# Kernel optimization log

Hardware: AMD Instinct MI355X
Metric: run time of the kernel (lower is better)

Reference implementation:

```python
import jax, jax.numpy as jnp
import numpy as np
from jax import lax

D_MODEL, D_STATE, DT_RANK, D_INNER, K = 96, 16, 6, 192, 4


def cross_scan(x):
    # x: (B, C, H, W) -> (B, 4, C, L)
    B, C, H, W = x.shape
    x0 = x.reshape(B, C, H * W)                         # row-major scan
    x1 = jnp.transpose(x, (0, 1, 3, 2)).reshape(B, C, H * W)  # column-major scan
    return jnp.stack([x0, x1, x0[..., ::-1], x1[..., ::-1]], axis=1)


def cross_merge(ys, H, W):
    # ys: (B, 4, D, L) -> (B, D, L)
    B, Kd, D, L = ys.shape
    ys = ys[:, 0:2] + ys[:, 2:4, :, ::-1]
    y1 = jnp.transpose(ys[:, 1].reshape(B, D, W, H), (0, 1, 3, 2)).reshape(B, D, L)
    return ys[:, 0] + y1


def selective_scan(u, delta, A, Bs, Cs, Ds, delta_bias):
    # u, delta: (B, K, D, L); A: (K, D, N); Bs, Cs: (B, K, N, L); Ds, delta_bias: (K, D)
    Bsz, Kd, Dm, L = u.shape
    N = A.shape[-1]
    delta = jax.nn.softplus(delta + delta_bias[None, :, :, None])
    du = delta * u
    d_l = jnp.moveaxis(delta, -1, 0)   # (L, B, K, D)
    du_l = jnp.moveaxis(du, -1, 0)
    b_l = jnp.moveaxis(Bs, -1, 0)      # (L, B, K, N)
    c_l = jnpp = jnp.moveaxis(Cs, -1, 0)

    def step(h, inp):
        d_t, du_t, b_t, c_t = inp
        h = jnp.exp(d_t[..., None] * A) * h + du_t[..., None] * b_t[:, :, None, :]
        y = jnp.einsum('bkdn,bkn->bkd', h, c_t)
        return h, y

    h0 = jnp.zeros((Bsz, Kd, Dm, N), u.dtype)
    _, ys = lax.scan(step, h0, (d_l, du_l, b_l, c_l))
    ys = jnp.moveaxis(ys, 0, -1)  # (B, K, D, L)
    return ys + Ds[None, :, :, None] * u


def _forward(x, in_proj_w, conv_w, conv_b, x_proj_w, dt_projs_w, dt_projs_b,
             A_logs, Ds, out_norm_w, out_norm_b, out_proj_w):
    Bsz, H, W, dm = x.shape
    d_in = conv_w.shape[0]
    R, N = dt_projs_w.shape[2], A_logs.shape[-1]
    L = H * W
    # in_proj (no bias), split into x and gate z
    xz = jnp.einsum('bhwc,oc->bhwo', x, in_proj_w)
    xpart, z = jnp.split(xz, 2, axis=-1)
    z = jax.nn.silu(z)
    # depthwise 3x3 conv (NCHW) + SiLU
    xc = jnp.transpose(xpart, (0, 3, 1, 2))
    xc = lax.conv_general_dilated(xc, conv_w, (1, 1), 'SAME',
                                  feature_group_count=d_in,
                                  dimension_numbers=('NCHW', 'OIHW', 'NCHW'))
    xc = jax.nn.silu(xc + conv_b[None, :, None, None])
    # 4-directional cross scan
    xs = cross_scan(xc)                                   # (B, 4, d_in, L)
    x_dbl = jnp.einsum('bkdl,kcd->bkcl', xs, x_proj_w)    # (B, 4, R+2N, L)
    dts = jnp.einsum('bkrl,kdr->bkdl', x_dbl[:, :, :R], dt_projs_w)
    Bs = x_dbl[:, :, R:R + N]
    Cs = x_dbl[:, :, R + N:]
    A = -jnp.exp(A_logs)                                  # (4, d_in, N)
    ys = selective_scan(xs, dts, A, Bs, Cs, Ds, dt_projs_b)
    y = cross_merge(ys, H, W)                             # (B, d_in, L)
    y = jnp.transpose(y.reshape(Bsz, d_in, H, W), (0, 2, 3, 1))
    # out_norm = LayerNorm(d_inner), eps=1e-5
    mu = y.mean(-1, keepdims=True)
    var = ((y - mu) ** 2).mean(-1, keepdims=True)
    y = (y - mu) / jnp.sqrt(var + 1e-5) * out_norm_w + out_norm_b
    y = y * z
    return jnp.einsum('bhwd,od->bhwo', y, out_proj_w)


def setup_inputs() -> dict:
    key = jax.random.key(0)
    ks = jax.random.split(key, 8)
    dm, d_in, N, R = D_MODEL, D_INNER, D_STATE, DT_RANK
    x = jax.random.normal(ks[0], (8, 64, 64, dm), jnp.float32)
    in_proj_w = jax.random.normal(ks[1], (2 * d_in, dm), jnp.float32) * 0.02
    conv_w = jax.random.normal(ks[2], (d_in, 1, 3, 3), jnp.float32) * 0.1
    conv_b = jnp.zeros((d_in,), jnp.float32)
    x_proj_w = jax.random.normal(ks[3], (K, R + 2 * N, d_in), jnp.float32) * 0.02
    dt_projs_w = jax.random.normal(ks[4], (K, d_in, R), jnp.float32) * 0.1
    dt_projs_b = jax.random.uniform(ks[5], (K, d_in), jnp.float32, minval=-4.0, maxval=-2.0)
    A_logs = jnp.log(jnp.tile(jnp.arange(1, N + 1, dtype=jnp.float32)[None, None, :], (K, d_in, 1)))
    Ds = jnp.ones((K, d_in), jnp.float32)
    out_norm_w = jnp.ones((d_in,), jnp.float32)
    out_norm_b = jnp.zeros((d_in,), jnp.float32)
    out_proj_w = jax.random.normal(ks[6], (dm, d_in), jnp.float32) * 0.02
    return dict(x=x, in_proj_w=in_proj_w, conv_w=conv_w, conv_b=conv_b,
                x_proj_w=x_proj_w, dt_projs_w=dt_projs_w, dt_projs_b=dt_projs_b,
                A_logs=A_logs, Ds=Ds, out_norm_w=out_norm_w, out_norm_b=out_norm_b,
                out_proj_w=out_proj_w)


def reference(x, in_proj_w, conv_w, conv_b, x_proj_w, dt_projs_w, dt_projs_b,
              A_logs, Ds, out_norm_w, out_norm_b, out_proj_w):
    return _forward(x, in_proj_w, conv_w, conv_b, x_proj_w, dt_projs_w, dt_projs_b,
                    A_logs, Ds, out_norm_w, out_norm_b, out_proj_w)
```

## Files before the change

### kernel.cpp

```cpp
#include <hip/hip_runtime.h>
#include <math.h>

#define B_SZ 8
#define Hh 64
#define Ww 64
#define L 4096
#define Dm 96
#define Din 192
#define Kd 4
#define Ns 16
#define CPROJ 38
#define ROWW 40
#define NCHUNK 128
#define CHUNK 32

__device__ __forceinline__ float siluf_(float x){ return x / (1.f + __expf(-x)); }

__global__ void prep_kernel(const float* __restrict__ inw,
                            const float* __restrict__ xpw,
                            const float* __restrict__ outw,
                            float* __restrict__ wt_in,
                            float* __restrict__ wt_x,
                            float* __restrict__ wt_out){
  int i = blockIdx.x * blockDim.x + threadIdx.x;
  if (i < Dm*2*Din){ int k = i/(2*Din); int o = i%(2*Din); wt_in[i] = inw[o*Dm + k]; }
  int j = i - Dm*2*Din;
  if (j >= 0 && j < Din*Kd*CPROJ){ int k = j/(Kd*CPROJ); int c = j%(Kd*CPROJ); wt_x[j] = xpw[c*Din + k]; }
  int l = j - Din*Kd*CPROJ;
  if (l >= 0 && l < Din*Dm){ int dd = l/Dm; int o = l%Dm; wt_out[l] = outw[o*Din + dd]; }
}

__global__ __launch_bounds__(256) void zero_kernel(float4* __restrict__ p, int n4){
  int i = blockIdx.x * 256 + threadIdx.x;
  if (i < n4) p[i] = make_float4(0.f,0.f,0.f,0.f);
}

template<int KDIM, int OREAL, int EPI>
__global__ __launch_bounds__(256) void gemm_kernel(const float* __restrict__ X,
    const float* __restrict__ W, float* __restrict__ out0, float* __restrict__ out1){
  __shared__ float4 xt[128*24];
  const int tid = threadIdx.x;
  const int pg = tid & 15, og = tid >> 4;
  const int pblk = blockIdx.x & 255;
  const int oblk = blockIdx.x >> 8;
  const int p0 = pblk * 128;
  const bool act = (oblk*128 + og*8) < OREAL;
  int oc = oblk*128 + og*8;
  if (oc > OREAL-8) oc = OREAL-8;
  const int sw = pg & 7;

  float acc[8][8];
  #pragma unroll
  for (int i=0;i<8;i++){
    #pragma unroll
    for (int j2=0;j2<8;j2++) acc[i][j2] = 0.f;
  }

  for (int kp = 0; kp < KDIM/96; ++kp){
    __syncthreads();
    for (int idx = tid; idx < 128*24; idx += 256){
      int pp = idx/24, k4 = idx%24;
      size_t prow;
      if (EPI == 1){
        int b = pblk >> 5, tau = pblk & 31;
        int h = ((tau>>2)<<3) + (pp>>4);
        int w = ((tau&3)<<4) + (pp&15);
        prow = (size_t)b*L + h*64 + w;
      } else prow = (size_t)p0 + pp;
      float4 v = *(const float4*)&X[prow*KDIM + (size_t)kp*96 + k4*4];
      xt[pp*24 + (k4 ^ (pp&7))] = v;
    }
    __syncthreads();

    if (act){
      for (int k4 = 0; k4 < 24; ++k4){
        float4 wv[8];
        #pragma unroll
        for (int kk=0;kk<4;kk++){
          const float* wr = &W[(size_t)(kp*96 + k4*4 + kk)*OREAL + oc];
          wv[kk*2]   = *(const float4*)wr;
          wv[kk*2+1] = *(const float4*)(wr+4);
        }
        float4 xv[8];
        #pragma unroll
        for (int i=0;i<8;i++) xv[i] = xt[(pg+16*i)*24 + (k4 ^ sw)];
        #pragma unroll
        for (int kk=0;kk<4;kk++){
          const float4 wa = wv[kk*2], wb = wv[kk*2+1];
          #pragma unroll
          for (int i=0;i<8;i++){
            const float xk = ((const float*)&xv[i])[kk];
            acc[i][0] += xk*wa.x; acc[i][1] += xk*wa.y; acc[i][2] += xk*wa.z; acc[i][3] += xk*wa.w;
            acc[i][4] += xk*wb.x; acc[i][5] += xk*wb.y; acc[i][6] += xk*wb.z; acc[i][7] += xk*wb.w;
          }
        }
      }
    }
  }

  if (!act) return;
  if (EPI == 0){
    #pragma unroll
    for (int i=0;i<8;i++){
      size_t p = (size_t)p0 + pg + 16*i;
      if (oc < Din){
        *(float4*)&out0[p*Din + oc]     = make_float4(acc[i][0],acc[i][1],acc[i][2],acc[i][3]);
        *(float4*)&out0[p*Din + oc + 4] = make_float4(acc[i][4],acc[i][5],acc[i][6],acc[i][7]);
      } else {
        int zo = oc - Din;
        *(float4*)&out1[p*Din + zo]     = make_float4(siluf_(acc[i][0]),siluf_(acc[i][1]),siluf_(acc[i][2]),siluf_(acc[i][3]));
        *(float4*)&out1[p*Din + zo + 4] = make_float4(siluf_(acc[i][4]),siluf_(acc[i][5]),siluf_(acc[i][6]),siluf_(acc[i][7]));
      }
    }
  } else if (EPI == 1){
    const int b = pblk >> 5, tau = pblk & 31;
    #pragma unroll
    for (int i=0;i<8;i++){
      int q = pg + 16*i;
      int h = ((tau>>2)<<3) + (q>>4);
      int w = ((tau&3)<<4) + (q&15);
      int hw = h*64 + w;
      int t1 = ((hw&63)<<6) | (hw>>6);
      #pragma unroll
      for (int j2=0;j2<8;j2++){
        int c = oc + j2;
        int kd = c / CPROJ; int cc = c - kd*CPROJ;
        int t = (kd==0)? hw : (kd==1)? t1 : (kd==2)? (L-1-hw) : (L-1-t1);
        int dcol = (cc < 6) ? (32+cc) : (cc-6);
        out0[((size_t)(b*Kd+kd)*L + t)*ROWW + dcol] = acc[i][j2];
      }
    }
  } else {
    #pragma unroll
    for (int i=0;i<8;i++){
      size_t p = (size_t)p0 + pg + 16*i;
      *(float4*)&out0[p*Dm + oc]     = make_float4(acc[i][0],acc[i][1],acc[i][2],acc[i][3]);
      *(float4*)&out0[p*Dm + oc + 4] = make_float4(acc[i][4],acc[i][5],acc[i][6],acc[i][7]);
    }
  }
}

__global__ __launch_bounds__(256) void conv_kernel(const float* __restrict__ xp,
    const float* __restrict__ cw, const float* __restrict__ cb, float* __restrict__ u){
  const int gid = blockIdx.x * 256 + threadIdx.x;
  const int d = gid % Din; const int p = gid / Din;
  const int b = p / L; const int hw = p % L; const int h = hw >> 6; const int w = hw & 63;
  float acc = cb[d];
  #pragma unroll
  for (int i=-1;i<=1;i++){
    const int hh = h + i; if (hh < 0 || hh >= Hh) continue;
    #pragma unroll
    for (int j=-1;j<=1;j++){
      const int ww = w + j; if (ww < 0 || ww >= Ww) continue;
      acc += xp[((size_t)(b*L + hh*Ww + ww))*Din + d] * cw[d*9 + (i+1)*3 + (j+1)];
    }
  }
  u[(size_t)p*Din + d] = siluf_(acc);
}

__device__ __forceinline__ void affine_pos(int k, int t0, int& gp0, int& gstr){
  if (k == 0){ gp0 = t0; gstr = 1; }
  else if (k == 1){ gp0 = ((t0 & 63) << 6) | (t0 >> 6); gstr = 64; }
  else if (k == 2){ gp0 = L-1-t0; gstr = -1; }
  else { const int T0 = L-1-t0; gp0 = ((T0 & 63) << 6) | (T0 >> 6); gstr = -64; }
}

__device__ __forceinline__ void ladder_(float e1, float* e){
  e[0]=e1;
  #pragma unroll
  for (int n=1;n<16;n++){ int P=n+1; e[n] = e[(P+1)/2 - 1] * e[P/2 - 1]; }
}

__device__ __forceinline__ float scan_step(const float* __restrict__ row, float uval,
    const float* __restrict__ wdt, float bias, const float* __restrict__ a2,
    bool fast, float* __restrict__ hst){
  float dr = bias;
  #pragma unroll
  for (int r=0;r<6;r++) dr += row[32+r]*wdt[r];
  const float p = __expf(dr);
  const float delta = (dr > 20.f) ? dr : __logf(1.f + p);
  const float du = delta * uval;
  float e[16];
  if (fast){
    ladder_(1.f/(1.f + p), e);
  } else {
    #pragma unroll
    for (int n=0;n<16;n++) e[n] = __expf(delta * a2[n]);
  }
  #pragma unroll
  for (int n=0;n<16;n++) hst[n] = e[n]*hst[n] + du*row[n];
  return delta;
}

__device__ __forceinline__ float ydot_(const float* __restrict__ hst,
    const float* __restrict__ row){
  float ya=0.f,yb=0.f,yc=0.f,yd=0.f;
  #pragma unroll
  for (int n=0;n<16;n+=4){
    ya += hst[n]*row[16+n];   yb += hst[n+1]*row[17+n];
    yc += hst[n+2]*row[18+n]; yd += hst[n+3]*row[19+n];
  }
  return (ya+yb)+(yc+yd);
}

__global__ __launch_bounds__(192) void scanq_kernel(const float* __restrict__ u,
    const float* __restrict__ xq, const float* __restrict__ dtw,
    const float* __restrict__ dtb, const float* __restrict__ alog,
    float* __restrict__ qout, float* __restrict__ Sout){
  const int bid = blockIdx.x;
  const int c = bid & (NCHUNK-1); const int k = (bid >> 7) & 3; const int b = bid >> 9;
  const int d = threadIdx.x;
  const int bk = b*Kd + k;
  float wdt[6];
  #pragma unroll
  for (int r=0;r<6;r++) wdt[r] = dtw[(k*Din + d)*6 + r];
  const float bias = dtb[k*Din + d];
  float a2[16]; bool fastb = true;
  #pragma unroll
  for (int n=0;n<16;n++){
    a2[n] = -__expf(alog[(k*Din + d)*16 + n]);
    fastb = fastb && (fabsf(a2[n] + (float)(n+1)) < 1e-5f*(float)(n+1));
  }
  const bool fast = (bool)__all((int)fastb);
  float hst[16];
  #pragma unroll
  for (int n=0;n<16;n++) hst[n] = 0.f;
  float S = 0.f;
  const int t0 = c * CHUNK;
  int gp0, gstr; affine_pos(k, t0, gp0, gstr);
  const float* __restrict__ up = u + (size_t)b*L*Din + (size_t)gp0*Din + d;
  const ptrdiff_t ustep = (ptrdiff_t)gstr * Din;
  const float* __restrict__ rowp = xq + ((size_t)bk*L + t0)*ROWW;
  for (int s = 0; s < CHUNK; ++s){
    S += scan_step(rowp, *up, wdt, bias, a2, fast, hst);
    up += ustep; rowp += ROWW;
  }
  const size_t base = ((size_t)bk*NCHUNK + c)*Ns*Din + d;
  #pragma unroll
  for (int n=0;n<16;n++) qout[base + (size_t)n*Din] = hst[n];
  Sout[((size_t)bk*NCHUNK + c)*Din + d] = S;
}

__global__ __launch_bounds__(256) void combine_kernel(const float* __restrict__ alog,
    float* __restrict__ q, const float* __restrict__ Sin){
  const int gid = blockIdx.x * 256 + threadIdx.x;
  if (gid >= B_SZ*Kd*Ns*Din) return;
  const int d = gid % Din; const int n = (gid / Din) % Ns; const int bk = gid / (Din*Ns);
  const int k = bk & 3;
  const float A = -__expf(alog[(k*Din + d)*16 + n]);
  float h = 0.f;
  for (int c=0;c<NCHUNK;c++){
    const size_t idx = (((size_t)bk*NCHUNK + c)*Ns + n)*Din + d;
    const float qv = q[idx];
    q[idx] = h;
    h = __expf(A * Sin[((size_t)bk*NCHUNK + c)*Din + d]) * h + qv;
  }
}

__global__ __launch_bounds__(192) void scany_kernel(const float* __restrict__ u,
    const float* __restrict__ xq, const float* __restrict__ dtw,
    const float* __restrict__ dtb, const float* __restrict__ alog,
    const float* __restrict__ Dsin, const float* __restrict__ hin,
    float* __restrict__ ym){
  const int bid = blockIdx.x;
  const int c = bid & (NCHUNK-1); const int k = (bid >> 7) & 3; const int b = bid >> 9;
  const int d = threadIdx.x;
  const int bk = b*Kd + k;

  float wdt[6];
  #pragma unroll
  for (int r=0;r<6;r++) wdt[r] = dtw[(k*Din + d)*6 + r];
  const float bias = dtb[k*Din + d];
  const float Dval = Dsin[k*Din + d];
  float a2[16]; bool fastb = true;
  #pragma unroll
  for (int n=0;n<16;n++){
    a2[n] = -__expf(alog[(k*Din + d)*16 + n]);
    fastb = fastb && (fabsf(a2[n] + (float)(n+1)) < 1e-5f*(float)(n+1));
  }
  const bool fast = (bool)__all((int)fastb);
  float hst[16];
  const size_t hbase = ((size_t)bk*NCHUNK + c)*Ns*Din + d;
  #pragma unroll
  for (int n=0;n<16;n++) hst[n] = hin[hbase + (size_t)n*Din];

  const int t0 = c * CHUNK;
  int gp0, gstr; affine_pos(k, t0, gp0, gstr);
  const float* __restrict__ up = u + (size_t)b*L*Din + (size_t)gp0*Din + d;
  float* __restrict__ yp = ym + (size_t)b*L*Din + (size_t)gp0*Din + d;
  const ptrdiff_t ustep = (ptrdiff_t)gstr * Din;
  const float* __restrict__ rowp = xq + ((size_t)bk*L + t0)*ROWW;
  for (int s = 0; s < CHUNK; ++s){
    const float uval = *up;
    scan_step(rowp, uval, wdt, bias, a2, fast, hst);
    atomicAdd(yp, ydot_(hst, rowp) + Dval*uval);
    up += ustep; yp += ustep; rowp += ROWW;
  }
}

__global__ __launch_bounds__(192) void lnz_kernel(const float* __restrict__ ym,
    const float* __restrict__ z,
    const float* __restrict__ gw, const float* __restrict__ gb,
    float* __restrict__ yg){
  __shared__ float red[2][4];
  const int p = blockIdx.x;
  const int d = threadIdx.x;
  const size_t i = (size_t)p*Din + d;
  const float yv = ym[i];
  float s = yv, ss = yv*yv;
  #pragma unroll
  for (int off=32; off>=1; off>>=1){ s += __shfl_down(s, off); ss += __shfl_down(ss, off); }
  const int wave = d >> 6;
  if ((d & 63) == 0){ red[0][wave] = s; red[1][wave] = ss; }
  __syncthreads();
  const float mu = (red[0][0]+red[0][1]+red[0][2]) * (1.f/Din);
  const float var = (red[1][0]+red[1][1]+red[1][2]) * (1.f/Din) - mu*mu;
  const float inv = rsqrtf(var + 1e-5f);
  yg[i] = ((yv - mu)*inv*gw[d] + gb[d]) * z[i];
}

extern "C" void kernel_launch(void* const* d_in, const int* in_sizes, int n_in,
                              void* d_out, int out_size, void* d_ws, size_t ws_size,
                              hipStream_t stream) {
  const float* x      = (const float*)d_in[0];
  const float* inw    = (const float*)d_in[1];
  const float* convw  = (const float*)d_in[2];
  const float* convb  = (const float*)d_in[3];
  const float* xprojw = (const float*)d_in[4];
  const float* dtw    = (const float*)d_in[5];
  const float* dtb    = (const float*)d_in[6];
  const float* alog   = (const float*)d_in[7];
  const float* Ds     = (const float*)d_in[8];
  const float* gw     = (const float*)d_in[9];
  const float* gb     = (const float*)d_in[10];
  const float* outw   = (const float*)d_in[11];
  float* out = (float*)d_out;

  float* ws = (float*)d_ws;
  const size_t nBLD  = (size_t)B_SZ*L*Din;
  const size_t nXQ   = (size_t)B_SZ*Kd*L*ROWW;
  const size_t nQ    = (size_t)B_SZ*Kd*NCHUNK*Ns*Din;
  const size_t nS    = (size_t)B_SZ*Kd*NCHUNK*Din;
  size_t off = 0;
  float* xpart = ws + off; off += nBLD;
  float* zbuf  = ws + off; off += nBLD;
  float* ubuf  = ws + off; off += nBLD;
  float* xq    = ws + off; off += nXQ;
  float* qbuf  = ws + off; off += nQ;
  float* Sbuf  = ws + off; off += nS;
  float* ym    = ws + off; off += nBLD;
  float* wt_in = ws + off; off += (size_t)Dm*2*Din;
  float* wt_x  = ws + off; off += (size_t)Din*Kd*CPROJ;
  float* wt_out= ws + off; off += (size_t)Din*Dm;

  const int prepN = Dm*2*Din + Din*Kd*CPROJ + Din*Dm;
  prep_kernel<<<(prepN + 255)/256, 256, 0, stream>>>(inw, xprojw, outw, wt_in, wt_x, wt_out);
  zero_kernel<<<(int)(nBLD/4 + 255)/256, 256, 0, stream>>>((float4*)ym, (int)(nBLD/4));
  gemm_kernel<Dm, 2*Din, 0><<<256*3, 256, 0, stream>>>(x, wt_in, xpart, zbuf);
  conv_kernel<<<(int)(nBLD/256), 256, 0, stream>>>(xpart, convw, convb, ubuf);
  gemm_kernel<Din, Kd*CPROJ, 1><<<256*2, 256, 0, stream>>>(ubuf, wt_x, xq, nullptr);
  scanq_kernel<<<B_SZ*Kd*NCHUNK, Din, 0, stream>>>(ubuf, xq, dtw, dtb, alog, qbuf, Sbuf);
  combine_kernel<<<(B_SZ*Kd*Ns*Din + 255)/256, 256, 0, stream>>>(alog, qbuf, Sbuf);
  scany_kernel<<<B_SZ*Kd*NCHUNK, Din, 0, stream>>>(ubuf, xq, dtw, dtb, alog, Ds, qbuf, ym);
  lnz_kernel<<<B_SZ*L, Din, 0, stream>>>(ym, zbuf, gw, gb, qbuf);
  gemm_kernel<Din, Dm, 2><<<256*1, 256, 0, stream>>>(qbuf, wt_out, out, nullptr);
}
```

Measured before the change: 501.4 us.

## Fuse layernorm-gate into out-projection kernel and vectorize scan row loads

Fuses the LayerNorm, z-gating and output projection into one kernel that stages normalized rows in swizzled shared memory, which removes the separate lnz pass and the intermediate buffer round trip. The scan kernels now load B/C/dt rows as float4 vectors, unroll the time loop and use a hardware reciprocal. The combine step writes prefix states to the reused xpart buffer instead of updating in place. The old scany_kernel is left with garbled, dead code that is never launched, and the workspace layout is resized to fit.

```diff
diff --git a/kernel.cpp b/kernel.cpp
--- a/kernel.cpp
+++ b/kernel.cpp
@@ -112,7 +112,7 @@
         *(float4*)&out1[p*Din + zo + 4] = make_float4(siluf_(acc[i][4]),siluf_(acc[i][5]),siluf_(acc[i][6]),siluf_(acc[i][7]));
       }
     }
-  } else if (EPI == 1){
+  } else {
     const int b = pblk >> 5, tau = pblk & 31;
     #pragma unroll
     for (int i=0;i<8;i++){
@@ -130,13 +130,6 @@
         out0[((size_t)(b*Kd+kd)*L + t)*ROWW + dcol] = acc[i][j2];
       }
     }
-  } else {
-    #pragma unroll
-    for (int i=0;i<8;i++){
-      size_t p = (size_t)p0 + pg + 16*i;
-      *(float4*)&out0[p*Dm + oc]     = make_float4(acc[i][0],acc[i][1],acc[i][2],acc[i][3]);
-      *(float4*)&out0[p*Dm + oc + 4] = make_float4(acc[i][4],acc[i][5],acc[i][6],acc[i][7]);
-    }
   }
 }
 
@@ -169,38 +162,6 @@
   e[0]=e1;
   #pragma unroll
   for (int n=1;n<16;n++){ int P=n+1; e[n] = e[(P+1)/2 - 1] * e[P/2 - 1]; }
-}
-
-__device__ __forceinline__ float scan_step(const float* __restrict__ row, float uval,
-    const float* __restrict__ wdt, float bias, const float* __restrict__ a2,
-    bool fast, float* __restrict__ hst){
-  float dr = bias;
-  #pragma unroll
-  for (int r=0;r<6;r++) dr += row[32+r]*wdt[r];
-  const float p = __expf(dr);
-  const float delta = (dr > 20.f) ? dr : __logf(1.f + p);
-  const float du = delta * uval;
-  float e[16];
-  if (fast){
-    ladder_(1.f/(1.f + p), e);
-  } else {
-    #pragma unroll
-    for (int n=0;n<16;n++) e[n] = __expf(delta * a2[n]);
-  }
-  #pragma unroll
-  for (int n=0;n<16;n++) hst[n] = e[n]*hst[n] + du*row[n];
-  return delta;
-}
-
-__device__ __forceinline__ float ydot_(const float* __restrict__ hst,
-    const float* __restrict__ row){
-  float ya=0.f,yb=0.f,yc=0.f,yd=0.f;
-  #pragma unroll
-  for (int n=0;n<16;n+=4){
-    ya += hst[n]*row[16+n];   yb += hst[n+1]*row[17+n];
-    yc += hst[n+2]*row[18+n]; yd += hst[n+3]*row[19+n];
-  }
-  return (ya+yb)+(yc+yd);
 }
 
 __global__ __launch_bounds__(192) void scanq_kernel(const float* __restrict__ u,
@@ -222,38 +183,59 @@
     fastb = fastb && (fabsf(a2[n] + (float)(n+1)) < 1e-5f*(float)(n+1));
   }
   const bool fast = (bool)__all((int)fastb);
-  float hst[16];
-  #pragma unroll
-  for (int n=0;n<16;n++) hst[n] = 0.f;
+  float h[16];
+  #pragma unroll
+  for (int n=0;n<16;n++) h[n] = 0.f;
   float S = 0.f;
   const int t0 = c * CHUNK;
   int gp0, gstr; affine_pos(k, t0, gp0, gstr);
   const float* __restrict__ up = u + (size_t)b*L*Din + (size_t)gp0*Din + d;
   const ptrdiff_t ustep = (ptrdiff_t)gstr * Din;
   const float* __restrict__ rowp = xq + ((size_t)bk*L + t0)*ROWW;
+  #pragma unroll 4
   for (int s = 0; s < CHUNK; ++s){
-    S += scan_step(rowp, *up, wdt, bias, a2, fast, hst);
+    const float4* __restrict__ rq = (const float4*)rowp;
+    const float4 B0=rq[0],B1=rq[1],B2=rq[2],B3=rq[3];
+    const float4 D0=rq[8];
+    const float2 D1=((const float2*)rowp)[18];
+    const float uval = *up;
+    float dr = bias + D0.x*wdt[0]+D0.y*wdt[1]+D0.z*wdt[2]+D0.w*wdt[3]+D1.x*wdt[4]+D1.y*wdt[5];
+    const float pp = __expf(dr);
+    const float delta = (dr > 20.f) ? dr : __logf(1.f + pp);
+    S += delta;
+    const float du = delta * uval;
+    float e[16];
+    if (fast){
+      ladder_(__builtin_amdgcn_rcpf(1.f + pp), e);
+    } else {
+      #pragma unroll
+      for (int n=0;n<16;n++) e[n] = __expf(delta * a2[n]);
+    }
+    h[0] =e[0] *h[0] +du*B0.x; h[1] =e[1] *h[1] +du*B0.y; h[2] =e[2] *h[2] +du*B0.z; h[3] =e[3] *h[3] +du*B0.w;
+    h[4] =e[4] *h[4] +du*B1.x; h[5] =e[5] *h[5] +du*B1.y; h[6] =e[6] *h[6] +du*B1.z; h[7] =e[7] *h[7] +du*B1.w;
+    h[8] =e[8] *h[8] +du*B2.x; h[9] =e[9] *h[9] +du*B2.y; h[10]=e[10]*h[10]+du*B2.z; h[11]=e[11]*h[11]+du*B2.w;
+    h[12]=e[12]*h[12]+du*B3.x; h[13]=e[13]*h[13]+du*B3.y; h[14]=e[14]*h[14]+du*B3.z; h[15]=e[15]*h[15]+du*B3.w;
     up += ustep; rowp += ROWW;
   }
   const size_t base = ((size_t)bk*NCHUNK + c)*Ns*Din + d;
   #pragma unroll
-  for (int n=0;n<16;n++) qout[base + (size_t)n*Din] = hst[n];
+  for (int n=0;n<16;n++) qout[base + (size_t)n*Din] = h[n];
   Sout[((size_t)bk*NCHUNK + c)*Din + d] = S;
 }
 
 __global__ __launch_bounds__(256) void combine_kernel(const float* __restrict__ alog,
-    float* __restrict__ q, const float* __restrict__ Sin){
+    const float* __restrict__ qin, const float* __restrict__ Sin, float* __restrict__ hout){
   const int gid = blockIdx.x * 256 + threadIdx.x;
   if (gid >= B_SZ*Kd*Ns*Din) return;
   const int d = gid % Din; const int n = (gid / Din) % Ns; const int bk = gid / (Din*Ns);
   const int k = bk & 3;
   const float A = -__expf(alog[(k*Din + d)*16 + n]);
   float h = 0.f;
+  #pragma unroll 2
   for (int c=0;c<NCHUNK;c++){
     const size_t idx = (((size_t)bk*NCHUNK + c)*Ns + n)*Din + d;
-    const float qv = q[idx];
-    q[idx] = h;
-    h = __expf(A * Sin[((size_t)bk*NCHUNK + c)*Din + d]) * h + qv;
+    hout[idx] = h;
+    h = __expf(A * Sin[((size_t)bk*NCHUNK + c)*Din + d]) * h + qin[idx];
   }
 }
 
@@ -279,10 +261,10 @@
     fastb = fastb && (fabsf(a2[n] + (float)(n+1)) < 1e-5f*(float)(n+1));
   }
   const bool fast = (bool)__all((int)fastb);
-  float hst[16];
+  float h[16];
   const size_t hbase = ((size_t)bk*NCHUNK + c)*Ns*Din + d;
   #pragma unroll
-  for (int n=0;n<16;n++) hst[n] = hin[hbase + (size_t)n*Din];
+  for (int n=0;n<16;n++) h[n] = hin[hbase + (size_t)n*Din];
 
   const int t0 = c * CHUNK;
   int gp0, gstr; affine_pos(k, t0, gp0, gstr);
@@ -290,33 +272,175 @@
   float* __restrict__ yp = ym + (size_t)b*L*Din + (size_t)gp0*Din + d;
   const ptrdiff_t ustep = (ptrdiff_t)gstr * Din;
   const float* __restrict__ rowp = xq + ((size_t)bk*L + t0)*ROWW;
+  #pragma unroll 4
   for (int s = 0; s < CHUNK; ++s){
+    const float4* __restrict__ rq = (const float4*)rowp;
+    const float4 B0=rq[0],B1=rq[1],B2=rq[2],B3=rq[3];
+    const float4 C0=rq[4],C1=rq[5],C2=rq[6],C3=rq[7];
+    const float4 D0=rq[8];
+    const float2 D1=((const float2*)rowp)[18];
     const float uval = *up;
-    scan_step(rowp, uval, wdt, bias, a2, fast, hst);
-    atomicAdd(yp, ydot_(hst, rowp) + Dval*uval);
+    float dr = bias + D0.x*wdt[0]+D0.y*wdt[1]+D0.z*wdt[2]+D0.w*wdt[3]+D1.x*wdt[4]+D1.y*wdt[5];
+    const float pp = __expf(dr);
+    const float delta = (dr > 20.f) ? dr : __logf(1.f + pp);
+    const float du = delta * uval;
+    float e[16];
+    if (fast){
+      ladder_(__builtin_amdgcn_rcpf(1.f + pp), e);
+    } else {
+      #pragma unroll
+      for (int n=0;n<16;n++) e[n] = __expf(delta * a2[n]);
+    }
+    h[0] =e[0] *h[0] +du*B0.x; h[1] =e[1] *h[1] +du*B0.y; h[2] =e[2] *h[2] +du*B0.z; h[3] =e[3] *h[3] +du*B0.w;
+    h[4] =e[4] *h[4] +du*B1.x; h[5] =e[5] *h[5] +du*B1.y; h[6] =e[6] *h[6] +du*B1.z; h[7] =e[7] *h[7] +du*B1.w;
+    h[8] =e[8] *h[8] +du*B2.x; h[9] =e[9] *h[9] +du*B2.z==0.f?h[9]:e[9]*h[9]+du*B2.y;
+    h[9] =e[9] *h[9];
     up += ustep; yp += ustep; rowp += ROWW;
   }
 }
 
-__global__ __launch_bounds__(192) void lnz_kernel(const float* __restrict__ ym,
-    const float* __restrict__ z,
-    const float* __restrict__ gw, const float* __restrict__ gb,
-    float* __restrict__ yg){
-  __shared__ float red[2][4];
-  const int p = blockIdx.x;
+__global__ __launch_bounds__(192) void scany_kernel2(const float* __restrict__ u,
+    const float* __restrict__ xq, const float* __restrict__ dtw,
+    const float* __restrict__ dtb, const float* __restrict__ alog,
+    const float* __restrict__ Dsin, const float* __restrict__ hin,
+    float* __restrict__ ym){
+  const int bid = blockIdx.x;
+  const int c = bid & (NCHUNK-1); const int k = (bid >> 7) & 3; const int b = bid >> 9;
   const int d = threadIdx.x;
-  const size_t i = (size_t)p*Din + d;
-  const float yv = ym[i];
-  float s = yv, ss = yv*yv;
-  #pragma unroll
-  for (int off=32; off>=1; off>>=1){ s += __shfl_down(s, off); ss += __shfl_down(ss, off); }
-  const int wave = d >> 6;
-  if ((d & 63) == 0){ red[0][wave] = s; red[1][wave] = ss; }
+  const int bk = b*Kd + k;
+
+  float wdt[6];
+  #pragma unroll
+  for (int r=0;r<6;r++) wdt[r] = dtw[(k*Din + d)*6 + r];
+  const float bias = dtb[k*Din + d];
+  const float Dval = Dsin[k*Din + d];
+  float a2[16]; bool fastb = true;
+  #pragma unroll
+  for (int n=0;n<16;n++){
+    a2[n] = -__expf(alog[(k*Din + d)*16 + n]);
+    fastb = fastb && (fabsf(a2[n] + (float)(n+1)) < 1e-5f*(float)(n+1));
+  }
+  const bool fast = (bool)__all((int)fastb);
+  float h[16];
+  const size_t hbase = ((size_t)bk*NCHUNK + c)*Ns*Din + d;
+  #pragma unroll
+  for (int n=0;n<16;n++) h[n] = hin[hbase + (size_t)n*Din];
+
+  const int t0 = c * CHUNK;
+  int gp0, gstr; affine_pos(k, t0, gp0, gstr);
+  const float* __restrict__ up = u + (size_t)b*L*Din + (size_t)gp0*Din + d;
+  float* __restrict__ yp = ym + (size_t)b*L*Din + (size_t)gp0*Din + d;
+  const ptrdiff_t ustep = (ptrdiff_t)gstr * Din;
+  const float* __restrict__ rowp = xq + ((size_t)bk*L + t0)*ROWW;
+  #pragma unroll 4
+  for (int s = 0; s < CHUNK; ++s){
+    const float4* __restrict__ rq = (const float4*)rowp;
+    const float4 B0=rq[0],B1=rq[1],B2=rq[2],B3=rq[3];
+    const float4 C0=rq[4],C1=rq[5],C2=rq[6],C3=rq[7];
+    const float4 D0=rq[8];
+    const float2 D1=((const float2*)rowp)[18];
+    const float uval = *up;
+    float dr = bias + D0.x*wdt[0]+D0.y*wdt[1]+D0.z*wdt[2]+D0.w*wdt[3]+D1.x*wdt[4]+D1.y*wdt[5];
+    const float pp = __expf(dr);
+    const float delta = (dr > 20.f) ? dr : __logf(1.f + pp);
+    const float du = delta * uval;
+    float e[16];
+    if (fast){
+      ladder_(__builtin_amdgcn_rcpf(1.f + pp), e);
+    } else {
+      #pragma unroll
+      for (int n=0;n<16;n++) e[n] = __expf(delta * a2[n]);
+    }
+    h[0] =e[0] *h[0] +du*B0.x; h[1] =e[1] *h[1] +du*B0.y; h[2] =e[2] *h[2] +du*B0.z; h[3] =e[3] *h[3] +du*B0.w;
+    h[4] =e[4] *h[4] +du*B1.x; h[5] =e[5] *h[5] +du*B1.y; h[6] =e[6] *h[6] +du*B1.z; h[7] =e[7] *h[7] +du*B1.w;
+    h[8] =e[8] *h[8] +du*B2.x; h[9] =e[9] *h[9] +du*B2.y; h[10]=e[10]*h[10]+du*B2.z; h[11]=e[11]*h[11]+du*B2.w;
+    h[12]=e[12]*h[12]+du*B3.x; h[13]=e[13]*h[13]+du*B3.y; h[14]=e[14]*h[14]+du*B3.z; h[15]=e[15]*h[15]+du*B3.w;
+    float y0 = h[0]*C0.x + h[1]*C0.y;  float y1 = h[2]*C0.z + h[3]*C0.w;
+    float y2 = h[4]*C1.x + h[5]*C1.y;  float y3 = h[6]*C1.z + h[7]*C1.w;
+    y0 += h[8]*C2.x + h[9]*C2.y;   y1 += h[10]*C2.z + h[11]*C2.w;
+    y2 += h[12]*C3.x + h[13]*C3.y; y3 += h[14]*C3.z + h[15]*C3.w;
+    atomicAdd(yp, (y0+y1)+(y2+y3) + Dval*uval);
+    up += ustep; yp += ustep; rowp += ROWW;
+  }
+}
+
+__global__ __launch_bounds__(192) void outproj_kernel(const float* __restrict__ ym,
+    const float* __restrict__ z, const float* __restrict__ gw, const float* __restrict__ gb,
+    const float* __restrict__ wto,
+    float* __restrict__ out){
+  __shared__ float xt[64*192];
+  __shared__ float smu[64], sinv[64];
+  const int tid = threadIdx.x;
+  const int p0 = blockIdx.x * 64;
+  if (tid < 128){
+    const int r = tid >> 1, part = tid & 1;
+    const float4* __restrict__ src = (const float4*)(ym + (size_t)(p0 + r)*Din + part*96);
+    float s = 0.f, ss = 0.f;
+    #pragma unroll
+    for (int i=0;i<24;i++){
+      float4 v = src[i];
+      s  += (v.x+v.y)+(v.z+v.w);
+      ss += (v.x*v.x+v.y*v.y)+(v.z*v.z+v.w*v.w);
+    }
+    s += __shfl_xor(s, 1); ss += __shfl_xor(ss, 1);
+    if (!part){
+      const float mu = s * (1.f/Din);
+      smu[r] = mu;
+      sinv[r] = rsqrtf(ss*(1.f/Din) - mu*mu + 1e-5f);
+    }
+  }
   __syncthreads();
-  const float mu = (red[0][0]+red[0][1]+red[0][2]) * (1.f/Din);
-  const float var = (red[1][0]+red[1][1]+red[1][2]) * (1.f/Din) - mu*mu;
-  const float inv = rsqrtf(var + 1e-5f);
-  yg[i] = ((yv - mu)*inv*gw[d] + gb[d]) * z[i];
+  for (int idx = tid; idx < 64*48; idx += 192){
+    const int r = idx/48, k4 = idx - (idx/48)*48;
+    const size_t g = (size_t)(p0+r)*Din + k4*4;
+    float4 v  = *(const float4*)(ym + g);
+    const float4 zv = *(const float4*)(z + g);
+    const float4 gwv = *(const float4*)(gw + k4*4);
+    const float4 gbv = *(const float4*)(gb + k4*4);
+    const float mu = smu[r], inv = sinv[r];
+    v.x = ((v.x-mu)*inv*gwv.x + gbv.x)*zv.x;
+    v.y = ((v.y-mu)*inv*gwv.y + gbv.y)*zv.y;
+    v.z = ((v.z-mu)*inv*gwv.z + gbv.z)*zv.z;
+    v.w = ((v.w-mu)*inv*gwv.w + gbv.w)*zv.w;
+    const int k4s = (k4 & ~7) | ((k4 ^ r) & 7);
+    *(float4*)(xt + r*192 + k4s*4) = v;
+  }
+  __syncthreads();
+  const int pg = tid/12, og = tid - (tid/12)*12;
+  const int oc = og*8;
+  float acc[4][8];
+  #pragma unroll
+  for (int i=0;i<4;i++){
+    #pragma unroll
+    for (int j=0;j<8;j++) acc[i][j] = 0.f;
+  }
+  for (int k4 = 0; k4 < 48; ++k4){
+    float4 xv[4];
+    #pragma unroll
+    for (int i=0;i<4;i++){
+      const int r = pg*4+i;
+      const int k4s = (k4 & ~7) | ((k4 ^ r) & 7);
+      xv[i] = *(const float4*)(xt + r*192 + k4s*4);
+    }
+    #pragma unroll
+    for (int j=0;j<4;j++){
+      const int k = k4*4 + j;
+      const float4 w0 = *(const float4*)(wto + (size_t)k*Dm + oc);
+      const float4 w1 = *(const float4*)(wto + (size_t)k*Dm + oc + 4);
+      #pragma unroll
+      for (int i=0;i<4;i++){
+        const float xk = ((const float*)&xv[i])[j];
+        acc[i][0] += xk*w0.x; acc[i][1] += xk*w0.y; acc[i][2] += xk*w0.z; acc[i][3] += xk*w0.w;
+        acc[i][4] += xk*w1.x; acc[i][5] += xk*w1.y; acc[i][6] += xk*w1.z; acc[i][7] += xk*w1.w;
+      }
+    }
+  }
+  #pragma unroll
+  for (int i=0;i<4;i++){
+    const size_t row = (size_t)p0 + pg*4 + i;
+    *(float4*)(out + row*Dm + oc)     = make_float4(acc[i][0],acc[i][1],acc[i][2],acc[i][3]);
+    *(float4*)(out + row*Dm + oc + 4) = make_float4(acc[i][4],acc[i][5],acc[i][6],acc[i][7]);
+  }
 }
 
 extern "C" void kernel_launch(void* const* d_in, const int* in_sizes, int n_in,
@@ -342,7 +466,7 @@
   const size_t nQ    = (size_t)B_SZ*Kd*NCHUNK*Ns*Din;
   const size_t nS    = (size_t)B_SZ*Kd*NCHUNK*Din;
   size_t off = 0;
-  float* xpart = ws + off; off += nBLD;
+  float* xpart = ws + off; off += nQ;
   float* zbuf  = ws + off; off += nBLD;
   float* ubuf  = ws + off; off += nBLD;
   float* xq    = ws + off; off += nXQ;
@@ -360,8 +484,7 @@
   conv_kernel<<<(int)(nBLD/256), 256, 0, stream>>>(xpart, convw, convb, ubuf);
   gemm_kernel<Din, Kd*CPROJ, 1><<<256*2, 256, 0, stream>>>(ubuf, wt_x, xq, nullptr);
   scanq_kernel<<<B_SZ*Kd*NCHUNK, Din, 0, stream>>>(ubuf, xq, dtw, dtb, alog, qbuf, Sbuf);
-  combine_kernel<<<(B_SZ*Kd*Ns*Din + 255)/256, 256, 0, stream>>>(alog, qbuf, Sbuf);
-  scany_kernel<<<B_SZ*Kd*NCHUNK, Din, 0, stream>>>(ubuf, xq, dtw, dtb, alog, Ds, qbuf, ym);
-  lnz_kernel<<<B_SZ*L, Din, 0, stream>>>(ym, zbuf, gw, gb, qbuf);
-  gemm_kernel<Din, Dm, 2><<<256*1, 256, 0, stream>>>(qbuf, wt_out, out, nullptr);
-}
+  combine_kernel<<<(B_SZ*Kd*Ns*Din + 255)/256, 256, 0, stream>>>(alog, qbuf, Sbuf, xpart);
+  scany_kernel2<<<B_SZ*Kd*NCHUNK, Din, 0, stream>>>(ubuf, xq, dtw, dtb, alog, Ds, xpart, ym);
+  outproj_kernel<<<B_SZ*L/64, 192, 0, stream>>>(ym, zbuf, gw, gb, wt_out, out);
+}
```

Measured after the change: 470.9 us. -6.1%, faster.
